# Optimization experiments

Measured on AMD Instinct MI355X. Metric: run time of the kernel, lower is better.

The kernel has to match this reference:

```python
import jax, jax.numpy as jnp
import numpy as np

B, C, V = 65536, 2, 3          # batch of coords, coord_dim, value_dim
D, K, S = 64, 1024, 4          # latent_dim, num_codes, num_latent_vectors (VQ stages)
H, L, F = 1024, 5, 25          # hidden_size, num_layers, num_freqs
IN = C * (2 * F + 1)           # 102: positional-encoded decoder input
COMMIT = 0.25


def setup_inputs() -> dict:
    key = jax.random.key(0)
    ks = jax.random.split(key, 12)
    coords = jax.random.uniform(ks[0], (B, C), jnp.float32, -1.0, 1.0)
    latents = jax.random.normal(ks[1], (1, S, D), jnp.float32)
    cb = jax.random.normal(ks[2], (S, K, D), jnp.float32)
    codebooks = cb / jnp.linalg.norm(cb, axis=-1, keepdims=True)  # unit-norm init as in module
    mod_W = jax.random.normal(ks[3], (L, D, H), jnp.float32) / np.sqrt(D)
    mod_b = jax.random.normal(ks[4], (L, H), jnp.float32) * 0.01
    dec_W0 = jax.random.normal(ks[5], (IN, H), jnp.float32) / np.sqrt(IN)
    dec_b0 = jax.random.normal(ks[6], (H,), jnp.float32) * 0.01
    dec_Wh = jax.random.normal(ks[7], (L - 1, H, H), jnp.float32) / np.sqrt(H)
    dec_bh = jax.random.normal(ks[8], (L - 1, H), jnp.float32) * 0.01
    dec_Wout = jax.random.normal(ks[9], (H, V), jnp.float32) / np.sqrt(H)
    dec_bout = jax.random.normal(ks[10], (V,), jnp.float32) * 0.01
    return dict(coords=coords, latent_idx=0, latents=latents, codebooks=codebooks,
                mod_W=mod_W, mod_b=mod_b, dec_W0=dec_W0, dec_b0=dec_b0,
                dec_Wh=dec_Wh, dec_bh=dec_bh, dec_Wout=dec_Wout, dec_bout=dec_bout)


def _vq(z, emb):
    # z: (1, D), emb: (K, D) -> squared-distance argmin + straight-through
    d = jnp.sum(z * z, axis=1, keepdims=True) - 2.0 * (z @ emb.T) + jnp.sum(emb * emb, axis=1)
    idx = jnp.argmin(d, axis=1)               # (1,)
    z_q = emb[idx]                            # (1, D)
    z_q_st = z_q + jax.lax.stop_gradient(z - z_q)   # fwd value == z, grad flows to embedding
    loss = COMMIT * jnp.mean((jax.lax.stop_gradient(z_q) - z) ** 2)
    return z_q_st, idx, loss


def reference(coords, latent_idx, latents, codebooks, mod_W, mod_b,
              dec_W0, dec_b0, dec_Wh, dec_bh, dec_Wout, dec_bout):
    img = latents[latent_idx]                 # (S, D)
    z_q_sum = jnp.zeros((1, D), coords.dtype)
    residual_target = jnp.zeros((1, D), coords.dtype)
    total_vq_loss = 0.0
    idxs = []
    for s in range(S):                        # residual VQ over fixed small #stages
        z_stage = img[s:s + 1]
        if s == 0:
            residual_target = z_stage
            z_cur = z_stage
        else:
            residual_target = residual_target + z_stage
            z_cur = residual_target - jax.lax.stop_gradient(z_q_sum)
        z_q_st, idx, l = _vq(z_cur, codebooks[s])
        z_q_sum = z_q_sum + z_q_st
        total_vq_loss = total_vq_loss + l
        idxs.append(idx)
    # modulation betas from the (same-for-all-rows) quantized latent; broadcast over B
    betas = jnp.einsum('od,ldh->loh', z_q_sum, mod_W) + mod_b[:, None, :]   # (L, 1, H)
    # positional encoding: [x, sin(pi*f0*x), cos(pi*f0*x), sin(pi*f1*x), ...]
    freqs = 2.0 ** jnp.arange(F, dtype=coords.dtype)
    ang = coords[:, None, :] * (freqs[None, :, None] * jnp.pi)              # (B, F, C)
    pe = jnp.concatenate(
        [coords, jnp.stack([jnp.sin(ang), jnp.cos(ang)], axis=2).reshape(coords.shape[0], -1)],
        axis=-1)                                                            # (B, IN)
    h = jax.nn.relu(pe @ dec_W0 + dec_b0 + betas[0])
    for i in range(L - 1):
        h = jax.nn.relu(h @ dec_Wh[i] + dec_bh[i] + betas[i + 1])
    values = h @ dec_Wout + dec_bout                                        # (B, V)
    return values, jnp.stack(idxs), total_vq_loss
```

## Files before the change

### kernel.cpp

```cpp
#include <hip/hip_runtime.h>
#include <hip/hip_bf16.h>
#include <stdint.h>

#define NB   65536
#define NC   2
#define NV   3
#define ND   64
#define NK   1024
#define NS   4
#define NH   1024
#define NL   5
#define NF   25
#define NIN  102
#define K0P  128

typedef float f32x4 __attribute__((ext_vector_type(4)));
typedef int   i32x4 __attribute__((ext_vector_type(4)));
typedef int   i32x8 __attribute__((ext_vector_type(8)));
typedef unsigned char u8;

__device__ __forceinline__ void load_lds16(const void* g, void* l) {
    __builtin_amdgcn_global_load_lds(
        (const __attribute__((address_space(1))) void*)g,
        (__attribute__((address_space(3))) void*)l,
        16, 0, 0);
}

__device__ __forceinline__ u8 to_fp8(float x) {
    return (u8)(__builtin_amdgcn_cvt_pk_fp8_f32(x, 0.0f, 0, false) & 0xff);
}

__global__ __launch_bounds__(1024) void vq_kernel(
    const float* __restrict__ latents, const int* __restrict__ latent_idx,
    const float* __restrict__ codebooks, float* __restrict__ zq_out,
    float* __restrict__ out) {
    __shared__ float zcur[ND], resid[ND], zqsum[ND], ssq[ND];
    __shared__ float sDw[16];
    __shared__ int   sKw[16];
    __shared__ int   sBest;
    int t = threadIdx.x, lane = t & 63, wv = t >> 6;
    const float* img = latents + (size_t)latent_idx[0] * (NS * ND);
    if (t < ND) { resid[t] = 0.f; zqsum[t] = 0.f; }
    __syncthreads();
    float lossAcc = 0.f;
    for (int s = 0; s < NS; s++) {
        if (t < ND) {
            float iv = img[s * ND + t];
            float r  = resid[t] + iv;
            resid[t] = r;
            zcur[t]  = (s == 0) ? iv : (r - zqsum[t]);
        }
        __syncthreads();
        float zz = 0.f;
#pragma unroll
        for (int d = 0; d < ND; d++) { float z = zcur[d]; zz += z * z; }
        const float4* e4 = (const float4*)(codebooks + ((size_t)s * NK + t) * ND);
        float dot = 0.f, ee = 0.f;
#pragma unroll
        for (int i = 0; i < 16; i++) {
            float4 v = e4[i];
            dot += zcur[4 * i + 0] * v.x; dot += zcur[4 * i + 1] * v.y;
            dot += zcur[4 * i + 2] * v.z; dot += zcur[4 * i + 3] * v.w;
            ee  += v.x * v.x; ee += v.y * v.y; ee += v.z * v.z; ee += v.w * v.w;
        }
        float dmin = zz - 2.0f * dot + ee;
        int   kmin = t;
#pragma unroll
        for (int m = 1; m < 64; m <<= 1) {
            float d2 = __shfl_xor(dmin, m);
            int   k2 = __shfl_xor(kmin, m);
            if (d2 < dmin || (d2 == dmin && k2 < kmin)) { dmin = d2; kmin = k2; }
        }
        if (lane == 0) { sDw[wv] = dmin; sKw[wv] = kmin; }
        __syncthreads();
        if (t == 0) {
            float bd = sDw[0]; int bk = sKw[0];
            for (int w = 1; w < 16; w++) {
                float d2 = sDw[w]; int k2 = sKw[w];
                if (d2 < bd || (d2 == bd && k2 < bk)) { bd = d2; bk = k2; }
            }
            sBest = bk;
            out[NB * NV + s] = (float)bk;
        }
        __syncthreads();
        int best = sBest;
        const float* eb = codebooks + ((size_t)s * NK + best) * ND;
        if (t < ND) {
            float zq = eb[t];
            float d  = zq - zcur[t];
            ssq[t]   = d * d;
            zqsum[t] = zqsum[t] + (zq + (zcur[t] - zq));
        }
        __syncthreads();
        if (t == 0) {
            float sum = 0.f;
            for (int d = 0; d < ND; d++) sum += ssq[d];
            lossAcc += 0.25f * (sum / (float)ND);
        }
    }
    if (t < ND) zq_out[t] = zqsum[t];
    if (t == 0) out[NB * NV + NS] = lossAcc;
}

__global__ __launch_bounds__(256) void betas_kernel(
    const float* __restrict__ zq, const float* __restrict__ mod_W,
    const float* __restrict__ mod_b, const float* __restrict__ b0,
    const float* __restrict__ bh, float* __restrict__ bb) {
    int g = blockIdx.x * 256 + threadIdx.x;
    int l = g >> 10, n = g & 1023;
    float acc = mod_b[g];
    for (int d = 0; d < ND; d++) acc += zq[d] * mod_W[(size_t)(l * ND + d) * NH + n];
    acc += (l == 0) ? b0[n] : bh[(size_t)(l - 1) * NH + n];
    bb[g] = acc;
}

__global__ __launch_bounds__(256) void init_out_kernel(
    const float* __restrict__ bout, float* __restrict__ out) {
    int g = blockIdx.x * 256 + threadIdx.x;
    out[g] = bout[g % NV];
}

__global__ __launch_bounds__(256) void prep_kernel(
    const float* __restrict__ src, u8* __restrict__ dst, int Ks, int Kp) {
    __shared__ float tile[32][33];
    src += (size_t)blockIdx.z * Ks * NH;
    dst += (size_t)blockIdx.z * NH * Kp;
    int k0 = blockIdx.x * 32, n0 = blockIdx.y * 32;
    int tx = threadIdx.x, ty = threadIdx.y;
    for (int i = 0; i < 4; i++) {
        int k = k0 + ty + i * 8;
        int n = n0 + tx;
        tile[ty + i * 8][tx] = (k < Ks) ? src[(size_t)k * NH + n] : 0.0f;
    }
    __syncthreads();
    for (int i = 0; i < 4; i++) {
        int n = n0 + ty + i * 8;
        int k = k0 + tx;
        dst[(size_t)n * Kp + k] = to_fp8(tile[tx][ty + i * 8] * 64.0f);
    }
}

__device__ __forceinline__ float pe_val(const float* coords, int m, int k) {
    if (k < 2) return coords[m * 2 + k];
    if (k >= NIN) return 0.0f;
    int u = k - 2;
    int f = u >> 2, r = u & 3;
    float c = coords[m * 2 + (r & 1)];
    float a = c * __builtin_ldexpf(3.14159274101257324f, f);
    return (r < 2) ? sinf(a) : cosf(a);
}

__global__ __launch_bounds__(256) void pe_kernel(
    const float* __restrict__ coords, u8* __restrict__ pe) {
    int g = blockIdx.x * 256 + threadIdx.x;
    int m = g >> 5, k4 = (g & 31) * 4;
    float v0 = pe_val(coords, m, k4 + 0);
    float v1 = pe_val(coords, m, k4 + 1);
    float v2 = pe_val(coords, m, k4 + 2);
    float v3 = pe_val(coords, m, k4 + 3);
    int p = __builtin_amdgcn_cvt_pk_fp8_f32(v0, v1, 0, false);
    p     = __builtin_amdgcn_cvt_pk_fp8_f32(v2, v3, p, true);
    ((int*)pe)[g] = p;
}

template <int MODE, int KT>
__global__ __launch_bounds__(256, 2) void gemm_kernel(
    const u8* __restrict__ A, const u8* __restrict__ W,
    const float* __restrict__ bb, u8* __restrict__ O,
    const float* __restrict__ Wout, float* __restrict__ out, int Mb) {
    __shared__ __align__(16) u8 smem[49152];
    u8* sA = smem;
    u8* sW = smem + 32768;
    int t   = threadIdx.x;
    int fid = blockIdx.x;
    int xcd = fid & 7;
    int j8  = fid >> 3;
    int bn  = j8 & 7;
    int bm  = xcd * (Mb >> 3) + (j8 >> 3);
    int lane = t & 63, wm = t >> 6;
    int q    = lane >> 4, r16 = lane & 15;
    int s2   = (r16 >> 1) & 3, par = r16 & 1;
    int plo  = par * 4 + (q ^ s2);
    int phi  = (par ^ 1) * 4 + (q ^ s2);

    f32x4 acc[4][8];
    f32x4 zero = {0.f, 0.f, 0.f, 0.f};
    for (int i = 0; i < 4; i++)
        for (int j = 0; j < 8; j++) acc[i][j] = zero;

#pragma unroll 1
    for (int it = 0; it < (KT >> 7); it++) {
        int kb = it << 7;
#pragma unroll
        for (int p = 0; p < 8; p++) {
            int g = p * 256 + t;
            int r = g >> 3, P = g & 7;
            int c = (((P & 3) ^ ((r >> 1) & 3)) << 1) | ((P >> 2) ^ (r & 1));
            load_lds16((const void*)(A + (size_t)(bm * 256 + r) * KT + kb + c * 16),
                       (void*)(sA + g * 16));
        }
#pragma unroll
        for (int p = 0; p < 4; p++) {
            int g = p * 256 + t;
            int r = g >> 3, P = g & 7;
            int c = (((P & 3) ^ ((r >> 1) & 3)) << 1) | ((P >> 2) ^ (r & 1));
            load_lds16((const void*)(W + (size_t)(bn * 128 + r) * KT + kb + c * 16),
                       (void*)(sW + g * 16));
        }
        __syncthreads();

        i32x8 bfr[8];
#pragma unroll
        for (int j = 0; j < 8; j++) {
            int base = (j * 16 + r16) * 128;
            i32x4 lo = *(const i32x4*)(sW + base + plo * 16);
            i32x4 hi = *(const i32x4*)(sW + base + phi * 16);
            bfr[j] = __builtin_shufflevector(lo, hi, 0, 1, 2, 3, 4, 5, 6, 7);
        }
#pragma unroll
        for (int i = 0; i < 4; i++) {
            int base = (wm * 64 + i * 16 + r16) * 128;
            i32x4 lo = *(const i32x4*)(sA + base + plo * 16);
            i32x4 hi = *(const i32x4*)(sA + base + phi * 16);
            i32x8 af = __builtin_shufflevector(lo, hi, 0, 1, 2, 3, 4, 5, 6, 7);
#pragma unroll
            for (int j = 0; j < 8; j++)
                acc[i][j] = __builtin_amdgcn_mfma_scale_f32_16x16x128_f8f6f4(
                    bfr[j], af, acc[i][j], 0, 0,
                    0, 0x79797979,
                    0, 0x7f7f7f7f);
        }
        __syncthreads();
    }

    if constexpr (MODE == 0) {
        u8* eb = smem;
        int ml = wm * 64 + r16;
#pragma unroll
        for (int i = 0; i < 4; i++) {
#pragma unroll
            for (int j = 0; j < 8; j++) {
                int nl = j * 16 + q * 4;
                f32x4 b4 = *(const f32x4*)(bb + bn * 128 + nl);
                float v0 = fmaxf(acc[i][j][0] + b4[0], 0.0f);
                float v1 = fmaxf(acc[i][j][1] + b4[1], 0.0f);
                float v2 = fmaxf(acc[i][j][2] + b4[2], 0.0f);
                float v3 = fmaxf(acc[i][j][3] + b4[3], 0.0f);
                int p = __builtin_amdgcn_cvt_pk_fp8_f32(v0, v1, 0, false);
                p     = __builtin_amdgcn_cvt_pk_fp8_f32(v2, v3, p, true);
                *(int*)(eb + (ml + i * 16) * 132 + nl) = p;
            }
        }
        __syncthreads();
#pragma unroll
        for (int rd = 0; rd < 8; rd++) {
            int g2  = rd * 256 + t;
            int row = g2 >> 3, cc = g2 & 7;
            i32x4 v = *(const i32x4*)(eb + row * 132 + cc * 16);
            *(i32x4*)(O + (size_t)(bm * 256 + row) * NH + bn * 128 + cc * 16) = v;
        }
    } else {
#pragma unroll
        for (int i = 0; i < 4; i++) {
            float p0 = 0.f, p1 = 0.f, p2 = 0.f;
#pragma unroll
            for (int j = 0; j < 8; j++) {
                int nb = bn * 128 + j * 16 + q * 4;
                f32x4 b4 = *(const f32x4*)(bb + nb);
#pragma unroll
                for (int r = 0; r < 4; r++) {
                    float val = fmaxf(acc[i][j][r] + b4[r], 0.0f);
                    const float* w = Wout + (size_t)(nb + r) * NV;
                    p0 += val * w[0]; p1 += val * w[1]; p2 += val * w[2];
                }
            }
            p0 += __shfl_xor(p0, 16); p0 += __shfl_xor(p0, 32);
            p1 += __shfl_xor(p1, 16); p1 += __shfl_xor(p1, 32);
            p2 += __shfl_xor(p2, 16); p2 += __shfl_xor(p2, 32);
            if (q == 0) {
                int m = bm * 256 + wm * 64 + i * 16 + r16;
                atomicAdd(&out[(size_t)m * NV + 0], p0);
                atomicAdd(&out[(size_t)m * NV + 1], p1);
                atomicAdd(&out[(size_t)m * NV + 2], p2);
            }
        }
    }
}

extern "C" void kernel_launch(void* const* d_in, const int* in_sizes, int n_in,
                              void* d_out, int out_size, void* d_ws, size_t ws_size,
                              hipStream_t stream) {
    const float* coords     = (const float*)d_in[0];
    const int*   latent_idx = (const int*)d_in[1];
    const float* latents    = (const float*)d_in[2];
    const float* codebooks  = (const float*)d_in[3];
    const float* mod_W      = (const float*)d_in[4];
    const float* mod_b      = (const float*)d_in[5];
    const float* dec_W0     = (const float*)d_in[6];
    const float* dec_b0     = (const float*)d_in[7];
    const float* dec_Wh     = (const float*)d_in[8];
    const float* dec_bh     = (const float*)d_in[9];
    const float* dec_Wout   = (const float*)d_in[10];
    const float* dec_bout   = (const float*)d_in[11];
    float* out = (float*)d_out;

    char* wsb = (char*)d_ws;
    float* zq  = (float*)(wsb + 0);
    float* bb  = (float*)(wsb + 256);
    u8*    W0T = (u8*)(wsb + 20736);
    u8*    WhT = (u8*)(wsb + 151808);
    const size_t fixed_end = 4346368;

    int Bc = 65536;
    while (Bc > 2048 && fixed_end + 2 * (size_t)Bc * NH > ws_size)
        Bc >>= 1;
    int Mb = Bc / 256;

    u8* hA = (u8*)(wsb + fixed_end);
    u8* hB = hA + (size_t)Bc * NH;
    u8* pe = hB;

    vq_kernel<<<1, 1024, 0, stream>>>(latents, latent_idx, codebooks, zq, out);
    betas_kernel<<<20, 256, 0, stream>>>(zq, mod_W, mod_b, dec_b0, dec_bh, bb);
    init_out_kernel<<<(NB * NV) / 256, 256, 0, stream>>>(dec_bout, out);
    prep_kernel<<<dim3(4, 32, 1), dim3(32, 8), 0, stream>>>(dec_W0, W0T, NIN, K0P);
    prep_kernel<<<dim3(32, 32, 4), dim3(32, 8), 0, stream>>>(dec_Wh, WhT, NH, NH);

    for (int c0 = 0; c0 < NB; c0 += Bc) {
        pe_kernel<<<(Bc * 32) / 256, 256, 0, stream>>>(coords + (size_t)c0 * NC, pe);
        gemm_kernel<0, K0P><<<8 * Mb, 256, 0, stream>>>(
            pe, W0T, bb + 0 * NH, hA, nullptr, nullptr, Mb);
        gemm_kernel<0, NH><<<8 * Mb, 256, 0, stream>>>(
            hA, WhT + 0 * (size_t)NH * NH, bb + 1 * NH, hB, nullptr, nullptr, Mb);
        gemm_kernel<0, NH><<<8 * Mb, 256, 0, stream>>>(
            hB, WhT + 1 * (size_t)NH * NH, bb + 2 * NH, hA, nullptr, nullptr, Mb);
        gemm_kernel<0, NH><<<8 * Mb, 256, 0, stream>>>(
            hA, WhT + 2 * (size_t)NH * NH, bb + 3 * NH, hB, nullptr, nullptr, Mb);
        gemm_kernel<1, NH><<<8 * Mb, 256, 0, stream>>>(
            hB, WhT + 3 * (size_t)NH * NH, bb + 4 * NH, nullptr,
            dec_Wout, out + (size_t)c0 * NV, Mb);
    }
}
```

Measured before the change: 516.3 us.

## Pre-swizzle operands into MFMA fragment layout and load directly from global

Weights, positional encodings and intermediate activations are now written in a blocked layout that matches the MFMA per-lane fragment order, so the GEMM kernel reads A and B fragments straight from global memory with 32-byte contiguous loads. The LDS staging, swizzled async copies and per-iteration barriers in the main loop are removed. LDS is kept only for the epilogue, which is cut to 32 KB. The cost is that operand reuse across waves now goes through L1/L2 instead of LDS, which adds global traffic and latency that is no longer hidden by explicit staging.

Measured after the change: 511.7 us. Within noise of the previous version (-0.9%).

```diff
diff --git a/kernel.cpp b/kernel.cpp
--- a/kernel.cpp
+++ b/kernel.cpp
@@ -19,16 +19,10 @@
 typedef int   i32x8 __attribute__((ext_vector_type(8)));
 typedef unsigned char u8;
 
-__device__ __forceinline__ void load_lds16(const void* g, void* l) {
-    __builtin_amdgcn_global_load_lds(
-        (const __attribute__((address_space(1))) void*)g,
-        (__attribute__((address_space(3))) void*)l,
-        16, 0, 0);
-}
-
 __device__ __forceinline__ u8 to_fp8(float x) {
     return (u8)(__builtin_amdgcn_cvt_pk_fp8_f32(x, 0.0f, 0, false) & 0xff);
 }
+
 
 __global__ __launch_bounds__(1024) void vq_kernel(
     const float* __restrict__ latents, const int* __restrict__ latent_idx,
@@ -123,6 +117,7 @@
 __global__ __launch_bounds__(256) void prep_kernel(
     const float* __restrict__ src, u8* __restrict__ dst, int Ks, int Kp) {
     __shared__ float tile[32][33];
+    int nIt = Kp >> 7;
     src += (size_t)blockIdx.z * Ks * NH;
     dst += (size_t)blockIdx.z * NH * Kp;
     int k0 = blockIdx.x * 32, n0 = blockIdx.y * 32;
@@ -133,10 +128,13 @@
         tile[ty + i * 8][tx] = (k < Ks) ? src[(size_t)k * NH + n] : 0.0f;
     }
     __syncthreads();
+    int it = k0 >> 7, q = (k0 >> 5) & 3;
     for (int i = 0; i < 4; i++) {
         int n = n0 + ty + i * 8;
         int k = k0 + tx;
-        dst[(size_t)n * Kp + k] = to_fp8(tile[tx][ty + i * 8] * 64.0f);
+        int bn = n >> 7, j = (n >> 4) & 7, r16 = n & 15;
+        size_t flat = ((size_t)(((bn * nIt + it) * 8 + j) * 64 + q * 16 + r16)) * 32 + tx;
+        dst[flat] = to_fp8(tile[tx][ty + i * 8] * 64.0f);
     }
 }
 
@@ -160,7 +158,8 @@
     float v3 = pe_val(coords, m, k4 + 3);
     int p = __builtin_amdgcn_cvt_pk_fp8_f32(v0, v1, 0, false);
     p     = __builtin_amdgcn_cvt_pk_fp8_f32(v2, v3, p, true);
-    ((int*)pe)[g] = p;
+    int m16 = m >> 4, r = m & 15, c32 = k4 >> 5, b = k4 & 31;
+    *(int*)(pe + ((size_t)(m16 * 4 + c32) * 16 + r) * 32 + b) = p;
 }
 
 template <int MODE, int KT>
@@ -168,9 +167,7 @@
     const u8* __restrict__ A, const u8* __restrict__ W,
     const float* __restrict__ bb, u8* __restrict__ O,
     const float* __restrict__ Wout, float* __restrict__ out, int Mb) {
-    __shared__ __align__(16) u8 smem[49152];
-    u8* sA = smem;
-    u8* sW = smem + 32768;
+    __shared__ __align__(16) u8 smem[32768];
     int t   = threadIdx.x;
     int fid = blockIdx.x;
     int xcd = fid & 7;
@@ -179,49 +176,31 @@
     int bm  = xcd * (Mb >> 3) + (j8 >> 3);
     int lane = t & 63, wm = t >> 6;
     int q    = lane >> 4, r16 = lane & 15;
-    int s2   = (r16 >> 1) & 3, par = r16 & 1;
-    int plo  = par * 4 + (q ^ s2);
-    int phi  = (par ^ 1) * 4 + (q ^ s2);
+    const int nIt = KT >> 7;
+
+    const u8* wbase = W + (size_t)(bn * nIt) * 16384 + lane * 32;
+    const u8* abase = A + ((size_t)(bm * 16 + wm * 4) * (KT >> 5)) * 512 + lane * 32;
 
     f32x4 acc[4][8];
     f32x4 zero = {0.f, 0.f, 0.f, 0.f};
     for (int i = 0; i < 4; i++)
         for (int j = 0; j < 8; j++) acc[i][j] = zero;
 
-#pragma unroll 1
-    for (int it = 0; it < (KT >> 7); it++) {
-        int kb = it << 7;
-#pragma unroll
-        for (int p = 0; p < 8; p++) {
-            int g = p * 256 + t;
-            int r = g >> 3, P = g & 7;
-            int c = (((P & 3) ^ ((r >> 1) & 3)) << 1) | ((P >> 2) ^ (r & 1));
-            load_lds16((const void*)(A + (size_t)(bm * 256 + r) * KT + kb + c * 16),
-                       (void*)(sA + g * 16));
-        }
-#pragma unroll
-        for (int p = 0; p < 4; p++) {
-            int g = p * 256 + t;
-            int r = g >> 3, P = g & 7;
-            int c = (((P & 3) ^ ((r >> 1) & 3)) << 1) | ((P >> 2) ^ (r & 1));
-            load_lds16((const void*)(W + (size_t)(bn * 128 + r) * KT + kb + c * 16),
-                       (void*)(sW + g * 16));
-        }
-        __syncthreads();
-
+#pragma unroll 2
+    for (int it = 0; it < nIt; it++) {
         i32x8 bfr[8];
 #pragma unroll
         for (int j = 0; j < 8; j++) {
-            int base = (j * 16 + r16) * 128;
-            i32x4 lo = *(const i32x4*)(sW + base + plo * 16);
-            i32x4 hi = *(const i32x4*)(sW + base + phi * 16);
+            const u8* p = wbase + (size_t)(it * 8 + j) * 2048;
+            i32x4 lo = *(const i32x4*)(p);
+            i32x4 hi = *(const i32x4*)(p + 16);
             bfr[j] = __builtin_shufflevector(lo, hi, 0, 1, 2, 3, 4, 5, 6, 7);
         }
 #pragma unroll
         for (int i = 0; i < 4; i++) {
-            int base = (wm * 64 + i * 16 + r16) * 128;
-            i32x4 lo = *(const i32x4*)(sA + base + plo * 16);
-            i32x4 hi = *(const i32x4*)(sA + base + phi * 16);
+            const u8* p = abase + ((size_t)i * (KT >> 5) + it * 4) * 512;
+            i32x4 lo = *(const i32x4*)(p);
+            i32x4 hi = *(const i32x4*)(p + 16);
             i32x8 af = __builtin_shufflevector(lo, hi, 0, 1, 2, 3, 4, 5, 6, 7);
 #pragma unroll
             for (int j = 0; j < 8; j++)
@@ -230,12 +209,10 @@
                     0, 0x79797979,
                     0, 0x7f7f7f7f);
         }
-        __syncthreads();
     }
 
     if constexpr (MODE == 0) {
         u8* eb = smem;
-        int ml = wm * 64 + r16;
 #pragma unroll
         for (int i = 0; i < 4; i++) {
 #pragma unroll
@@ -248,16 +225,19 @@
                 float v3 = fmaxf(acc[i][j][3] + b4[3], 0.0f);
                 int p = __builtin_amdgcn_cvt_pk_fp8_f32(v0, v1, 0, false);
                 p     = __builtin_amdgcn_cvt_pk_fp8_f32(v2, v3, p, true);
-                *(int*)(eb + (ml + i * 16) * 132 + nl) = p;
+                int idx = (((wm * 4 + i) * 4 + (j >> 1)) * 16 + r16) * 32
+                        + (j & 1) * 16 + q * 4;
+                *(int*)(eb + idx) = p;
             }
         }
         __syncthreads();
 #pragma unroll
         for (int rd = 0; rd < 8; rd++) {
             int g2  = rd * 256 + t;
-            int row = g2 >> 3, cc = g2 & 7;
-            i32x4 v = *(const i32x4*)(eb + row * 132 + cc * 16);
-            *(i32x4*)(O + (size_t)(bm * 256 + row) * NH + bn * 128 + cc * 16) = v;
+            int seg = g2 >> 5, off = (g2 & 31) * 16;
+            int m16l = seg >> 2, c32l = seg & 3;
+            i32x4 v = *(const i32x4*)(eb + seg * 512 + off);
+            *(i32x4*)(O + ((size_t)((bm * 16 + m16l) * 32 + bn * 4 + c32l)) * 512 + off) = v;
         }
     } else {
 #pragma unroll
```
